# Performance work log

Hardware: AMD Instinct MI355X
Metric: run time of the kernel (lower is better)

The kernel has to match this reference:

```python
import jax, jax.numpy as jnp
from jax import lax
import numpy as np

D_MODEL = 1024
EXPAND = 2
D_INNER = D_MODEL * EXPAND
D_STATE = 16
D_CONV = 4
DECAY = 0.95
LN_EPS = 1e-5


def setup_inputs() -> dict:
    key = jax.random.key(0)
    ks = jax.random.split(key, 9)
    b, s = 4, 2048
    scale = 1.0 / np.sqrt(D_MODEL)
    inner_scale = 1.0 / np.sqrt(D_INNER)
    return {
        "x": jax.random.normal(ks[0], (b, s, D_MODEL), dtype=jnp.float32),
        "W_in": jax.random.normal(ks[1], (2 * D_INNER, D_MODEL), dtype=jnp.float32) * scale,
        "conv_w": jax.random.normal(ks[2], (D_INNER, 1, D_CONV), dtype=jnp.float32) * 0.5,
        "conv_b": jax.random.normal(ks[3], (D_INNER,), dtype=jnp.float32) * 0.1,
        "W_x": jax.random.normal(ks[4], (2 * D_STATE, D_INNER), dtype=jnp.float32) * inner_scale,
        "B_log": jax.random.normal(ks[5], (D_INNER, D_STATE), dtype=jnp.float32) * 0.05,  # xavier-ish small
        "W_out": jax.random.normal(ks[6], (D_MODEL, D_INNER), dtype=jnp.float32) * inner_scale,
        "ln_g": jnp.ones((D_MODEL,), dtype=jnp.float32),
        "ln_b": jnp.zeros((D_MODEL,), dtype=jnp.float32),
    }


def _ssm_block(x, W_in, conv_w, conv_b, W_x, B_log, W_out, ln_g, ln_b):
    b, s, _ = x.shape
    d_inner = W_in.shape[0] // 2
    d_conv = conv_w.shape[-1]

    # input projection and gate split
    xz = jnp.einsum('bsd,ed->bse', x, W_in)            # [b, s, 2*d_inner]
    x_inner, z = jnp.split(xz, 2, axis=-1)             # each [b, s, d_inner]

    # causal depthwise conv (left pad d_conv-1, output length s)
    xc = jnp.transpose(x_inner, (0, 2, 1))             # [b, d_inner, s]
    conv = lax.conv_general_dilated(
        xc, conv_w, window_strides=(1,), padding=[(d_conv - 1, 0)],
        feature_group_count=d_inner)
    conv = conv + conv_b[None, :, None]
    x_conv = jax.nn.silu(jnp.transpose(conv, (0, 2, 1)))  # [b, s, d_inner]

    # selective parameters; s_B is produced but unused in the original math
    sp = jnp.einsum('bsd,nd->bsn', x_conv, W_x)        # [b, s, 2*d_state]
    _s_B, s_C = jnp.split(sp, 2, axis=-1)              # each [b, s, d_state]

    B = jnp.exp(B_log)                                  # [d_inner, d_state]

    # state_t = 0.95*state_{t-1} + B * x_t  factorizes as  state = B[d,n]*h[b,t,d]
    # with h_t = 0.95*h_{t-1} + x_conv_t ; scan over time with [b, d_inner] carry.
    def step(h, xt):
        h = DECAY * h + xt
        return h, h

    h0 = jnp.zeros((b, d_inner), dtype=x.dtype)
    _, h = lax.scan(step, h0, jnp.swapaxes(x_conv, 0, 1))  # [s, b, d_inner]
    h = jnp.swapaxes(h, 0, 1)                              # [b, s, d_inner]

    # output_t[b,d] = sum_n state[b,d,n]*s_C[b,t,n] = h[b,t,d] * (s_C @ B^T)[b,t,d]
    y = h * jnp.einsum('bsn,dn->bsd', s_C, B)
    y = y * jax.nn.silu(z)
    y = jnp.einsum('bsd,od->bso', y, W_out)            # [b, s, d_model]

    resid = x + y
    mu = jnp.mean(resid, axis=-1, keepdims=True)
    var = jnp.var(resid, axis=-1, keepdims=True)
    return (resid - mu) * lax.rsqrt(var + LN_EPS) * ln_g + ln_b


def reference(x, W_in, conv_w, conv_b, W_x, B_log, W_out, ln_g, ln_b):
    return _ssm_block(x, W_in, conv_w, conv_b, W_x, B_log, W_out, ln_g, ln_b)
```

## Files before the change

### kernel.cpp

```cpp
#include <hip/hip_runtime.h>
#include <hip/hip_bf16.h>
#include <stdint.h>

#define DM   1024
#define DI   2048
#define NST  16
#define BSZ  4
#define SLEN 2048
#define MROWS (BSZ*SLEN)
#define CHUNK 32
#define NCH  (SLEN/CHUNK)
#define DECAYF 0.95f
#define MB (size_t)1048576

typedef _Float16 f16;
typedef __attribute__((ext_vector_type(2))) _Float16 f16x2;
typedef __attribute__((ext_vector_type(4))) _Float16 f16x4;
typedef __attribute__((ext_vector_type(8))) _Float16 f16x8;
typedef __attribute__((ext_vector_type(4))) float f32x4;

__device__ __forceinline__ float silu_f(float v) { return v / (1.f + __expf(-v)); }

__device__ __forceinline__ void gload16(const f16* lds, const f16* g) {
  __builtin_amdgcn_global_load_lds((const __attribute__((address_space(1))) void*)g,
                                   (__attribute__((address_space(3))) void*)lds, 16, 0, 0);
}

#define NX4  (MROWS * DM / 4)
#define NWI4 (2 * DI * DM / 4)
#define NWO4 (DM * DI / 4)
__global__ __launch_bounds__(256) void cvt_all(
    const float* __restrict__ x, const float* __restrict__ wi, const float* __restrict__ wo,
    f16* __restrict__ A1, f16* __restrict__ B1, f16* __restrict__ W2)
{
  int i = blockIdx.x * 256 + threadIdx.x;
  const float* src; f16* dst; int j;
  if (i < NX4)              { src = x;  dst = A1; j = i; }
  else if (i < NX4 + NWI4)  { src = wi; dst = B1; j = i - NX4; }
  else                      { src = wo; dst = W2; j = i - NX4 - NWI4; }
  float4 v = ((const float4*)src)[j];
  f16x4 o = {(f16)v.x, (f16)v.y, (f16)v.z, (f16)v.w};
  ((f16x4*)dst)[j] = o;
}

__global__ void expb_t(const float* __restrict__ B_log, float* __restrict__ expBT) {
  int i = blockIdx.x * blockDim.x + threadIdx.x;
  int n = i >> 11, d = i & (DI - 1);
  expBT[i] = __expf(B_log[d * NST + n]);
}

template<int MODE>
__global__ __launch_bounds__(256) void gemm_bt(
    const f16* __restrict__ A, const f16* __restrict__ Bt,
    int K, f16* __restrict__ O0, f16* __restrict__ O1)
{
  __shared__ __align__(16) f16 sA[128 * 64];
  __shared__ __align__(16) f16 sB[128 * 64];
  const int tid  = threadIdx.x;
  const int lane = tid & 63;
  const int w    = tid >> 6;
  const int wr   = w >> 1, wc = w & 1;

  const int nwg  = gridDim.x * gridDim.y;
  int wgid = blockIdx.y * gridDim.x + blockIdx.x;
  wgid = (wgid & 7) * (nwg >> 3) + (wgid >> 3);
  const int bx = wgid % gridDim.x;
  const int by = wgid / gridDim.x;

  const int mBase = by * 128;
  const int nBase = bx * 128;
  const int lr = lane & 15;
  const int lu = lane >> 4;

  f32x4 acc[4][4];
  #pragma unroll
  for (int m = 0; m < 4; ++m)
    #pragma unroll
    for (int n = 0; n < 4; ++n)
      acc[m][n] = (f32x4){0.f, 0.f, 0.f, 0.f};

  int offA[4][2], offB[4][2];
  #pragma unroll
  for (int m = 0; m < 4; ++m) {
    int ra = wr * 64 + m * 16 + lr;
    int rb = wc * 64 + m * 16 + lr;
    #pragma unroll
    for (int kk = 0; kk < 2; ++kk) {
      offA[m][kk] = ra * 64 + ((kk * 4 + lu) ^ (ra & 7)) * 8;
      offB[m][kk] = rb * 64 + ((kk * 4 + lu) ^ (rb & 7)) * 8;
    }
  }

  for (int k0 = 0; k0 < K; k0 += 64) {
    #pragma unroll
    for (int j = 0; j < 4; ++j) {
      int c = j * 256 + tid;
      int row = c >> 3, p = c & 7;
      int su = p ^ (row & 7);
      gload16(&sA[c * 8], A  + (size_t)(mBase + row) * K + k0 + su * 8);
      gload16(&sB[c * 8], Bt + (size_t)(nBase + row) * K + k0 + su * 8);
    }
    __syncthreads();
    #pragma unroll
    for (int kk = 0; kk < 2; ++kk) {
      f16x8 af[4], bf[4];
      #pragma unroll
      for (int m = 0; m < 4; ++m) af[m] = *(const f16x8*)&sA[offA[m][kk]];
      #pragma unroll
      for (int n = 0; n < 4; ++n) bf[n] = *(const f16x8*)&sB[offB[n][kk]];
      #pragma unroll
      for (int m = 0; m < 4; ++m)
        #pragma unroll
        for (int n = 0; n < 4; ++n)
          acc[m][n] = __builtin_amdgcn_mfma_f32_16x16x32_f16(af[m], bf[n], acc[m][n], 0, 0, 0);
    }
    __syncthreads();
  }

  const int rq = (lane >> 4) * 4;
  f16* sOut = sA;
  const bool isZ = (MODE == 1) && (nBase >= DI);
  f16* dst = (MODE == 0) ? O0 : (isZ ? O1 : O0);
  const int ncols = (MODE == 0) ? DM : DI;
  const int cb = isZ ? (nBase - DI) : nBase;
  #pragma unroll
  for (int m = 0; m < 4; ++m) {
    #pragma unroll
    for (int n = 0; n < 4; ++n)
      #pragma unroll
      for (int r = 0; r < 4; ++r)
        sOut[(wr * 16 + rq + r) * 128 + wc * 64 + n * 16 + lr] = (f16)acc[m][n][r];
    __syncthreads();
    #pragma unroll
    for (int q = 0; q < 2; ++q) {
      int cidx = q * 256 + tid;
      int orow = cidx >> 4;
      int ocol = (cidx & 15) * 8;
      int grow = mBase + (orow >> 4) * 64 + m * 16 + (orow & 15);
      f16x8 v = *(const f16x8*)&sOut[orow * 128 + ocol];
      *(f16x8*)&dst[(size_t)grow * ncols + cb + ocol] = v;
    }
    __syncthreads();
  }
}

__global__ __launch_bounds__(256) void conv_scan(
    const f16* __restrict__ Xi, const float* __restrict__ convW, const float* __restrict__ convB,
    f16* __restrict__ Xc, f16* __restrict__ Hl, float* __restrict__ L)
{
  const int tid = threadIdx.x;
  const int d0 = (blockIdx.x * 256 + tid) * 2;
  const int ch = blockIdx.y;
  const int b  = blockIdx.z;
  const int t0 = ch * CHUNK;

  float w0[2], w1[2], w2[2], w3[2], cb[2];
  #pragma unroll
  for (int i = 0; i < 2; ++i) {
    float4 wv = ((const float4*)convW)[d0 + i];
    w0[i] = wv.x; w1[i] = wv.y; w2[i] = wv.z; w3[i] = wv.w;
    cb[i] = convB[d0 + i];
  }

  auto loadrow = [&](int t, float* dst) {
    if (t < 0) { dst[0] = dst[1] = 0.f; return; }
    f16x2 v = *(const f16x2*)&Xi[((size_t)(b * SLEN + t)) * DI + d0];
    dst[0] = (float)v.x; dst[1] = (float)v.y;
  };

  float xm3[2], xm2[2], xm1[2];
  loadrow(t0 - 3, xm3); loadrow(t0 - 2, xm2); loadrow(t0 - 1, xm1);

  float h[2] = {0.f, 0.f};
  for (int t = 0; t < CHUNK; ++t) {
    const size_t ro = ((size_t)(b * SLEN + t0 + t)) * DI + d0;
    f16x2 xv = *(const f16x2*)&Xi[ro];
    float xt[2] = {(float)xv.x, (float)xv.y};
    float xc[2];
    #pragma unroll
    for (int i = 0; i < 2; ++i) {
      float c = cb[i] + w0[i]*xm3[i] + w1[i]*xm2[i] + w2[i]*xm1[i] + w3[i]*xt[i];
      xc[i] = silu_f(c);
      h[i] = DECAYF * h[i] + xc[i];
    }
    f16x2 xco = {(f16)xc[0], (f16)xc[1]};
    f16x2 hho = {(f16)h[0], (f16)h[1]};
    *(f16x2*)&Xc[ro] = xco;
    *(f16x2*)&Hl[ro] = hho;
    #pragma unroll
    for (int i = 0; i < 2; ++i) { xm3[i] = xm2[i]; xm2[i] = xm1[i]; xm1[i] = xt[i]; }
  }
  float2 lo = {h[0], h[1]};
  *(float2*)&L[((size_t)(b * NCH + ch)) * DI + d0] = lo;
}

__global__ void carry_scan(const float* __restrict__ L, float* __restrict__ Carry) {
  int i = blockIdx.x * blockDim.x + threadIdx.x;
  int b = i >> 11, d = i & (DI - 1);
  float dp = 1.f;
  #pragma unroll
  for (int k = 0; k < CHUNK; ++k) dp *= DECAYF;
  float c = 0.f;
  for (int ch0 = 0; ch0 < NCH; ch0 += 8) {
    float lv[8];
    #pragma unroll
    for (int k = 0; k < 8; ++k)
      lv[k] = L[((size_t)(b * NCH + ch0 + k)) * DI + d];
    #pragma unroll
    for (int k = 0; k < 8; ++k) {
      c = dp * c + lv[k];
      Carry[((size_t)(b * NCH + ch0 + k)) * DI + d] = c;
    }
  }
}

__global__ __launch_bounds__(256) void sc_gemm(const f16* __restrict__ Xc, const float* __restrict__ Wx,
                                               float* __restrict__ sC) {
  const int m = blockIdx.x * 4 + (threadIdx.x >> 6);
  const int lane = threadIdx.x & 63;
  float acc[16];
  #pragma unroll
  for (int n = 0; n < 16; ++n) acc[n] = 0.f;
  #pragma unroll
  for (int it = 0; it < DI / 256; ++it) {
    int d = it * 256 + lane * 4;
    f16x4 xv = *(const f16x4*)&Xc[(size_t)m * DI + d];
    float x0 = (float)xv.x, x1 = (float)xv.y, x2 = (float)xv.z, x3 = (float)xv.w;
    #pragma unroll
    for (int n = 0; n < 16; ++n) {
      float4 wv = *(const float4*)&Wx[(size_t)(16 + n) * DI + d];
      acc[n] += x0 * wv.x + x1 * wv.y + x2 * wv.z + x3 * wv.w;
    }
  }
  #pragma unroll
  for (int n = 0; n < 16; ++n) {
    #pragma unroll
    for (int off = 32; off > 0; off >>= 1) acc[n] += __shfl_xor(acc[n], off);
  }
  if (lane == 0) {
    #pragma unroll
    for (int n = 0; n < 16; ++n) sC[m * 16 + n] = acc[n];
  }
}

__global__ __launch_bounds__(256) void ew_y(
    const f16* __restrict__ Hl, const f16* __restrict__ Zs,
    const float* __restrict__ sC, const float* __restrict__ expBT,
    const float* __restrict__ Carry, f16* __restrict__ Y)
{
  const int r = threadIdx.x >> 6, lane = threadIdx.x & 63;
  const int m = blockIdx.y * 4 + r;
  const int d0 = blockIdx.x * 512 + lane * 8;
  const int b = m >> 11, t = m & (SLEN - 1);
  const int ch = t / CHUNK, tl = t & (CHUNK - 1);

  float coef = 0.f;
  if (ch > 0) {
    coef = 1.f;
    for (int j = 0; j <= tl; ++j) coef *= DECAYF;
  }

  const float4 sc0 = *(const float4*)&sC[m * 16 + 0];
  const float4 sc1 = *(const float4*)&sC[m * 16 + 4];
  const float4 sc2 = *(const float4*)&sC[m * 16 + 8];
  const float4 sc3 = *(const float4*)&sC[m * 16 + 12];
  const float scv[16] = {sc0.x, sc0.y, sc0.z, sc0.w, sc1.x, sc1.y, sc1.z, sc1.w,
                         sc2.x, sc2.y, sc2.z, sc2.w, sc3.x, sc3.y, sc3.z, sc3.w};

  const size_t ro = (size_t)m * DI + d0;
  f16x8 hvv = *(const f16x8*)&Hl[ro];
  f16x8 zvv = *(const f16x8*)&Zs[ro];
  float hv[8], zv[8], ca[8];
  #pragma unroll
  for (int i = 0; i < 8; ++i) {
    hv[i] = (float)hvv[i];
    zv[i] = silu_f((float)zvv[i]);
    ca[i] = 0.f;
  }
  if (ch > 0) {
    const size_t co = ((size_t)(b * NCH + ch - 1)) * DI + d0;
    float4 c0 = *(const float4*)&Carry[co];
    float4 c1 = *(const float4*)&Carry[co + 4];
    ca[0] = c0.x; ca[1] = c0.y; ca[2] = c0.z; ca[3] = c0.w;
    ca[4] = c1.x; ca[5] = c1.y; ca[6] = c1.z; ca[7] = c1.w;
  }

  float cp[8] = {0.f, 0.f, 0.f, 0.f, 0.f, 0.f, 0.f, 0.f};
  #pragma unroll
  for (int n = 0; n < 16; ++n) {
    float4 e0 = *(const float4*)&expBT[(size_t)n * DI + d0];
    float4 e1 = *(const float4*)&expBT[(size_t)n * DI + d0 + 4];
    cp[0] += scv[n] * e0.x; cp[1] += scv[n] * e0.y; cp[2] += scv[n] * e0.z; cp[3] += scv[n] * e0.w;
    cp[4] += scv[n] * e1.x; cp[5] += scv[n] * e1.y; cp[6] += scv[n] * e1.z; cp[7] += scv[n] * e1.w;
  }

  f16x8 o;
  #pragma unroll
  for (int i = 0; i < 8; ++i) {
    float y = (hv[i] + coef * ca[i]) * cp[i] * zv[i];
    o[i] = (f16)y;
  }
  *(f16x8*)&Y[ro] = o;
}

__global__ __launch_bounds__(256) void ln_res(const f16* __restrict__ G, const float* __restrict__ x,
                                              const float* __restrict__ lng, const float* __restrict__ lnb,
                                              float* __restrict__ out) {
  const int m = blockIdx.x;
  const int tid = threadIdx.x;
  f16x4 gv4 = ((const f16x4*)(G + (size_t)m * DM))[tid];
  float4 xv = ((const float4*)(x + (size_t)m * DM))[tid];
  float4 rv = {(float)gv4.x + xv.x, (float)gv4.y + xv.y, (float)gv4.z + xv.z, (float)gv4.w + xv.w};
  float s = rv.x + rv.y + rv.z + rv.w;
  float s2 = rv.x * rv.x + rv.y * rv.y + rv.z * rv.z + rv.w * rv.w;
  #pragma unroll
  for (int off = 32; off > 0; off >>= 1) {
    s += __shfl_xor(s, off);
    s2 += __shfl_xor(s2, off);
  }
  __shared__ float ps[8];
  const int w = tid >> 6;
  if ((tid & 63) == 0) { ps[w] = s; ps[w + 4] = s2; }
  __syncthreads();
  float S = ps[0] + ps[1] + ps[2] + ps[3];
  float S2 = ps[4] + ps[5] + ps[6] + ps[7];
  float mu = S * (1.f / DM);
  float var = S2 * (1.f / DM) - mu * mu;
  float rs = rsqrtf(var + 1e-5f);
  float4 gg = ((const float4*)lng)[tid];
  float4 bb = ((const float4*)lnb)[tid];
  float4 ov = {(rv.x - mu) * rs * gg.x + bb.x, (rv.y - mu) * rs * gg.y + bb.y,
               (rv.z - mu) * rs * gg.z + bb.z, (rv.w - mu) * rs * gg.w + bb.w};
  ((float4*)(out + (size_t)m * DM))[tid] = ov;
}

extern "C" void kernel_launch(void* const* d_in, const int* in_sizes, int n_in,
                              void* d_out, int out_size, void* d_ws, size_t ws_size,
                              hipStream_t stream) {
  const float* x      = (const float*)d_in[0];
  const float* W_in   = (const float*)d_in[1];
  const float* conv_w = (const float*)d_in[2];
  const float* conv_b = (const float*)d_in[3];
  const float* W_x    = (const float*)d_in[4];
  const float* B_log  = (const float*)d_in[5];
  const float* W_out  = (const float*)d_in[6];
  const float* ln_g   = (const float*)d_in[7];
  const float* ln_b   = (const float*)d_in[8];
  float* out = (float*)d_out;

  char* ws = (char*)d_ws;
  f16*   Xi  = (f16*)(ws + 0);
  f16*   Yp  = (f16*)(ws + 0);
  f16*   Zs  = (f16*)(ws + 32 * MB);
  f16*   Xc  = (f16*)(ws + 64 * MB);
  f16*   Hl  = (f16*)(ws + 96 * MB);
  f16*   A1  = (f16*)(ws + 128 * MB);
  f16*   B1  = (f16*)(ws + 144 * MB);
  f16*   W2  = (f16*)(ws + 152 * MB);
  f16*   G   = (f16*)(ws + 156 * MB);
  float* L     = (float*)(ws + 172 * MB);
  float* Carry = (float*)(ws + 174 * MB);
  float* sC    = (float*)(ws + 176 * MB);
  float* expBT = (float*)(ws + 177 * MB);

  cvt_all<<<(NX4 + NWI4 + NWO4) / 256, 256, 0, stream>>>(x, W_in, W_out, A1, B1, W2);
  expb_t<<<(NST * DI) / 256, 256, 0, stream>>>(B_log, expBT);

  gemm_bt<1><<<dim3(2 * DI / 128, MROWS / 128), 256, 0, stream>>>(A1, B1, DM, Xi, Zs);

  conv_scan<<<dim3(DI / 512, NCH, BSZ), 256, 0, stream>>>(Xi, conv_w, conv_b, Xc, Hl, L);
  carry_scan<<<(BSZ * DI) / 256, 256, 0, stream>>>(L, Carry);
  sc_gemm<<<MROWS / 4, 256, 0, stream>>>(Xc, W_x, sC);
  ew_y<<<dim3(DI / 512, MROWS / 4), 256, 0, stream>>>(Hl, Zs, sC, expBT, Carry, Yp);

  gemm_bt<0><<<dim3(DM / 128, MROWS / 128), 256, 0, stream>>>(Yp, W2, DI, G, nullptr);

  ln_res<<<MROWS, 256, 0, stream>>>(G, x, ln_g, ln_b, out);
}
```

Before: 268.5 us.

## Recompute conv+silu inside sc_gemm, fold expB into cvt, store carry as f16

Stops conv_scan from writing the x_conv tensor and instead recomputes the causal depthwise conv and SiLU inside sc_gemm from the four neighbouring Xi rows. The aim is to save a 32 MB write and read. It also merges the exp(B_log) transpose into the conversion kernel to drop one launch, and stores the chunk carries in fp16 to halve that traffic. The cost is that sc_gemm now does four row loads plus the conv and SiLU maths per element, though the neighbouring rows should mostly hit in cache. Storing carries in fp16 lowers their precision.

After: 429.9 us. 60.1% more time.

```diff
diff --git a/kernel.cpp b/kernel.cpp
--- a/kernel.cpp
+++ b/kernel.cpp
@@ -29,24 +29,29 @@
 #define NX4  (MROWS * DM / 4)
 #define NWI4 (2 * DI * DM / 4)
 #define NWO4 (DM * DI / 4)
+#define NE4  (NST * DI / 4)
 __global__ __launch_bounds__(256) void cvt_all(
     const float* __restrict__ x, const float* __restrict__ wi, const float* __restrict__ wo,
-    f16* __restrict__ A1, f16* __restrict__ B1, f16* __restrict__ W2)
+    const float* __restrict__ B_log,
+    f16* __restrict__ A1, f16* __restrict__ B1, f16* __restrict__ W2, float* __restrict__ expBT)
 {
   int i = blockIdx.x * 256 + threadIdx.x;
-  const float* src; f16* dst; int j;
-  if (i < NX4)              { src = x;  dst = A1; j = i; }
-  else if (i < NX4 + NWI4)  { src = wi; dst = B1; j = i - NX4; }
-  else                      { src = wo; dst = W2; j = i - NX4 - NWI4; }
-  float4 v = ((const float4*)src)[j];
-  f16x4 o = {(f16)v.x, (f16)v.y, (f16)v.z, (f16)v.w};
-  ((f16x4*)dst)[j] = o;
-}
-
-__global__ void expb_t(const float* __restrict__ B_log, float* __restrict__ expBT) {
-  int i = blockIdx.x * blockDim.x + threadIdx.x;
-  int n = i >> 11, d = i & (DI - 1);
-  expBT[i] = __expf(B_log[d * NST + n]);
+  if (i < NX4 + NWI4 + NWO4) {
+    const float* src; f16* dst; int j;
+    if (i < NX4)              { src = x;  dst = A1; j = i; }
+    else if (i < NX4 + NWI4)  { src = wi; dst = B1; j = i - NX4; }
+    else                      { src = wo; dst = W2; j = i - NX4 - NWI4; }
+    float4 v = ((const float4*)src)[j];
+    f16x4 o = {(f16)v.x, (f16)v.y, (f16)v.z, (f16)v.w};
+    ((f16x4*)dst)[j] = o;
+  } else {
+    int j = i - NX4 - NWI4 - NWO4;
+    int base = j * 4;
+    int n = base >> 11, d = base & (DI - 1);
+    float4 o = {__expf(B_log[(d + 0) * NST + n]), __expf(B_log[(d + 1) * NST + n]),
+                __expf(B_log[(d + 2) * NST + n]), __expf(B_log[(d + 3) * NST + n])};
+    ((float4*)expBT)[j] = o;
+  }
 }
 
 template<int MODE>
@@ -146,7 +151,7 @@
 
 __global__ __launch_bounds__(256) void conv_scan(
     const f16* __restrict__ Xi, const float* __restrict__ convW, const float* __restrict__ convB,
-    f16* __restrict__ Xc, f16* __restrict__ Hl, float* __restrict__ L)
+    f16* __restrict__ Hl, float* __restrict__ L)
 {
   const int tid = threadIdx.x;
   const int d0 = (blockIdx.x * 256 + tid) * 2;
@@ -176,16 +181,13 @@
     const size_t ro = ((size_t)(b * SLEN + t0 + t)) * DI + d0;
     f16x2 xv = *(const f16x2*)&Xi[ro];
     float xt[2] = {(float)xv.x, (float)xv.y};
-    float xc[2];
     #pragma unroll
     for (int i = 0; i < 2; ++i) {
       float c = cb[i] + w0[i]*xm3[i] + w1[i]*xm2[i] + w2[i]*xm1[i] + w3[i]*xt[i];
-      xc[i] = silu_f(c);
-      h[i] = DECAYF * h[i] + xc[i];
-    }
-    f16x2 xco = {(f16)xc[0], (f16)xc[1]};
+      float xc = silu_f(c);
+      h[i] = DECAYF * h[i] + xc;
+    }
     f16x2 hho = {(f16)h[0], (f16)h[1]};
-    *(f16x2*)&Xc[ro] = xco;
     *(f16x2*)&Hl[ro] = hho;
     #pragma unroll
     for (int i = 0; i < 2; ++i) { xm3[i] = xm2[i]; xm2[i] = xm1[i]; xm1[i] = xt[i]; }
@@ -194,7 +196,7 @@
   *(float2*)&L[((size_t)(b * NCH + ch)) * DI + d0] = lo;
 }
 
-__global__ void carry_scan(const float* __restrict__ L, float* __restrict__ Carry) {
+__global__ void carry_scan(const float* __restrict__ L, f16* __restrict__ Carry) {
   int i = blockIdx.x * blockDim.x + threadIdx.x;
   int b = i >> 11, d = i & (DI - 1);
   float dp = 1.f;
@@ -209,27 +211,44 @@
     #pragma unroll
     for (int k = 0; k < 8; ++k) {
       c = dp * c + lv[k];
-      Carry[((size_t)(b * NCH + ch0 + k)) * DI + d] = c;
-    }
-  }
-}
-
-__global__ __launch_bounds__(256) void sc_gemm(const f16* __restrict__ Xc, const float* __restrict__ Wx,
-                                               float* __restrict__ sC) {
+      Carry[((size_t)(b * NCH + ch0 + k)) * DI + d] = (f16)c;
+    }
+  }
+}
+
+__global__ __launch_bounds__(256) void sc_gemm(
+    const f16* __restrict__ Xi, const float* __restrict__ convW, const float* __restrict__ convB,
+    const float* __restrict__ Wx, float* __restrict__ sC)
+{
   const int m = blockIdx.x * 4 + (threadIdx.x >> 6);
   const int lane = threadIdx.x & 63;
+  const int b = m >> 11, t = m & (SLEN - 1);
+  const f16* rowt = Xi + ((size_t)(b * SLEN + t)) * DI;
+
   float acc[16];
   #pragma unroll
   for (int n = 0; n < 16; ++n) acc[n] = 0.f;
+
   #pragma unroll
   for (int it = 0; it < DI / 256; ++it) {
     int d = it * 256 + lane * 4;
-    f16x4 xv = *(const f16x4*)&Xc[(size_t)m * DI + d];
-    float x0 = (float)xv.x, x1 = (float)xv.y, x2 = (float)xv.z, x3 = (float)xv.w;
+    f16x4 zz = {(f16)0, (f16)0, (f16)0, (f16)0};
+    f16x4 x0 = *(const f16x4*)&rowt[d];
+    f16x4 x1 = (t >= 1) ? *(const f16x4*)&rowt[d - DI]     : zz;
+    f16x4 x2 = (t >= 2) ? *(const f16x4*)&rowt[d - 2 * DI] : zz;
+    f16x4 x3 = (t >= 3) ? *(const f16x4*)&rowt[d - 3 * DI] : zz;
+    float xc[4];
+    #pragma unroll
+    for (int i = 0; i < 4; ++i) {
+      float4 wv = ((const float4*)convW)[d + i];
+      float c = convB[d + i] + wv.x * (float)x3[i] + wv.y * (float)x2[i]
+                             + wv.z * (float)x1[i] + wv.w * (float)x0[i];
+      xc[i] = silu_f(c);
+    }
     #pragma unroll
     for (int n = 0; n < 16; ++n) {
       float4 wv = *(const float4*)&Wx[(size_t)(16 + n) * DI + d];
-      acc[n] += x0 * wv.x + x1 * wv.y + x2 * wv.z + x3 * wv.w;
+      acc[n] += xc[0] * wv.x + xc[1] * wv.y + xc[2] * wv.z + xc[3] * wv.w;
     }
   }
   #pragma unroll
@@ -246,7 +265,7 @@
 __global__ __launch_bounds__(256) void ew_y(
     const f16* __restrict__ Hl, const f16* __restrict__ Zs,
     const float* __restrict__ sC, const float* __restrict__ expBT,
-    const float* __restrict__ Carry, f16* __restrict__ Y)
+    const f16* __restrict__ Carry, f16* __restrict__ Y)
 {
   const int r = threadIdx.x >> 6, lane = threadIdx.x & 63;
   const int m = blockIdx.y * 4 + r;
@@ -279,10 +298,9 @@
   }
   if (ch > 0) {
     const size_t co = ((size_t)(b * NCH + ch - 1)) * DI + d0;
-    float4 c0 = *(const float4*)&Carry[co];
-    float4 c1 = *(const float4*)&Carry[co + 4];
-    ca[0] = c0.x; ca[1] = c0.y; ca[2] = c0.z; ca[3] = c0.w;
-    ca[4] = c1.x; ca[5] = c1.y; ca[6] = c1.z; ca[7] = c1.w;
+    f16x8 cv = *(const f16x8*)&Carry[co];
+    #pragma unroll
+    for (int i = 0; i < 8; ++i) ca[i] = (float)cv[i];
   }
 
   float cp[8] = {0.f, 0.f, 0.f, 0.f, 0.f, 0.f, 0.f, 0.f};
@@ -352,25 +370,24 @@
   f16*   Xi  = (f16*)(ws + 0);
   f16*   Yp  = (f16*)(ws + 0);
   f16*   Zs  = (f16*)(ws + 32 * MB);
-  f16*   Xc  = (f16*)(ws + 64 * MB);
-  f16*   Hl  = (f16*)(ws + 96 * MB);
-  f16*   A1  = (f16*)(ws + 128 * MB);
-  f16*   B1  = (f16*)(ws + 144 * MB);
-  f16*   W2  = (f16*)(ws + 152 * MB);
-  f16*   G   = (f16*)(ws + 156 * MB);
-  float* L     = (float*)(ws + 172 * MB);
-  float* Carry = (float*)(ws + 174 * MB);
-  float* sC    = (float*)(ws + 176 * MB);
-  float* expBT = (float*)(ws + 177 * MB);
-
-  cvt_all<<<(NX4 + NWI4 + NWO4) / 256, 256, 0, stream>>>(x, W_in, W_out, A1, B1, W2);
-  expb_t<<<(NST * DI) / 256, 256, 0, stream>>>(B_log, expBT);
+  f16*   Hl  = (f16*)(ws + 64 * MB);
+  f16*   A1  = (f16*)(ws + 96 * MB);
+  f16*   B1  = (f16*)(ws + 112 * MB);
+  f16*   W2  = (f16*)(ws + 120 * MB);
+  f16*   G   = (f16*)(ws + 124 * MB);
+  float* L     = (float*)(ws + 140 * MB);
+  f16*   Carry = (f16*)(ws + 142 * MB);
+  float* sC    = (float*)(ws + 143 * MB);
+  float* expBT = (float*)(ws + 144 * MB);
+
+  cvt_all<<<(NX4 + NWI4 + NWO4 + NE4) / 256, 256, 0, stream>>>(
+      x, W_in, W_out, B_log, A1, B1, W2, expBT);
 
   gemm_bt<1><<<dim3(2 * DI / 128, MROWS / 128), 256, 0, stream>>>(A1, B1, DM, Xi, Zs);
 
-  conv_scan<<<dim3(DI / 512, NCH, BSZ), 256, 0, stream>>>(Xi, conv_w, conv_b, Xc, Hl, L);
+  conv_scan<<<dim3(DI / 512, NCH, BSZ), 256, 0, stream>>>(Xi, conv_w, conv_b, Hl, L);
   carry_scan<<<(BSZ * DI) / 256, 256, 0, stream>>>(L, Carry);
-  sc_gemm<<<MROWS / 4, 256, 0, stream>>>(Xc, W_x, sC);
+  sc_gemm<<<MROWS / 4, 256, 0, stream>>>(Xi, conv_w, conv_b, W_x, sC);
   ew_y<<<dim3(DI / 512, MROWS / 4), 256, 0, stream>>>(Hl, Zs, sC, expBT, Carry, Yp);
 
   gemm_bt<0><<<dim3(DM / 128, MROWS / 128), 256, 0, stream>>>(Yp, W2, DI, G, nullptr);
```
